# Optimization experiments

Hardware: AMD Instinct MI355X
Metric: run time of the kernel (lower is better)

Reference implementation:

```python
import jax, jax.numpy as jnp
import numpy as np

EPS = 1e-12  # matches torch.nn.functional.normalize default eps


def setup_inputs() -> dict:
    key = jax.random.key(0)
    k_x, k_org = jax.random.split(key)
    batch, times, d = 32, 256, 2048
    x = jax.random.normal(k_x, (batch, d, d), dtype=jnp.float32)
    # org.data.normal_(mean=0, std=0.1)
    org = 0.1 * jax.random.normal(k_org, (times, d), dtype=jnp.float32)
    return {"x": x, "org": org}


def reference(x, org):
    # F.normalize(org, dim=-1): divide each row by max(||row||_2, eps)
    norm = jnp.linalg.norm(org, axis=-1, keepdims=True)
    o = org / jnp.maximum(norm, EPS)  # (times, d)
    # Original: m = o_a (x) o_a  (rank-1 projectors, (times,d,d));
    #           y = einsum('abc,dce->dabe', m, x); trace = einsum('abcc->ab', y)
    # Algebraically: trace[batch, time] = sum_{b,c} o[a,b] * o[a,c] * x[d,c,b]
    # i.e. the quadratic form o^T x^T o per (batch, time) pair -- same math,
    # without materializing the (batch, times, d, d) intermediate.
    trace = jnp.einsum('ab,ac,dcb->da', o, o, x)  # (batch, times)
    return trace
```

## Files before the change

### kernel.cpp

```cpp
#include <hip/hip_runtime.h>
#include <hip/hip_bf16.h>

#define DDIM 2048
#define TTIMES 256
#define NT 64
#define THREADS 512

typedef __attribute__((ext_vector_type(8))) short short8;
typedef __attribute__((ext_vector_type(4))) float f32x4;

using gvoid = const __attribute__((address_space(1))) void;
using svoid = __attribute__((address_space(3))) void;

__device__ __forceinline__ void gld16(const void* g, void* l) {
    __builtin_amdgcn_global_load_lds((gvoid*)g, (svoid*)l, 16, 0, 0);
}

__device__ __forceinline__ ushort f2bf(float f) {
    union { float f; unsigned int u; } v; v.f = f;
    unsigned int u = v.u;
    unsigned int r = (u + 0x7FFFu + ((u >> 16) & 1u)) >> 16;
    return (ushort)r;
}
__device__ __forceinline__ float bf2f(ushort u) {
    union { unsigned int u; float f; } v; v.u = ((unsigned int)u) << 16;
    return v.f;
}
__device__ __forceinline__ short cvt1(float f) {
    union { __hip_bfloat16 h; ushort u; } cv;
    cv.h = __float2bfloat16(f);
    return (short)cv.u;
}

__global__ void norm_rows(const float* __restrict__ org, ushort* __restrict__ obf) {
    const int a   = blockIdx.x;
    const int tid = threadIdx.x;
    const float* row = org + (size_t)a * DDIM;
    float4 v0 = ((const float4*)row)[tid * 2];
    float4 v1 = ((const float4*)row)[tid * 2 + 1];
    float s = v0.x*v0.x + v0.y*v0.y + v0.z*v0.z + v0.w*v0.w
            + v1.x*v1.x + v1.y*v1.y + v1.z*v1.z + v1.w*v1.w;
    #pragma unroll
    for (int off = 1; off < 64; off <<= 1) s += __shfl_xor(s, off);
    __shared__ float wsum[4];
    const int lane = tid & 63, w = tid >> 6;
    if (lane == 0) wsum[w] = s;
    __syncthreads();
    const float tot = wsum[0] + wsum[1] + wsum[2] + wsum[3];
    const float scale = 1.0f / fmaxf(sqrtf(tot), 1e-12f);
    union { ushort u[8]; uint4 v; } pk;
    pk.u[0] = f2bf(v0.x * scale); pk.u[1] = f2bf(v0.y * scale);
    pk.u[2] = f2bf(v0.z * scale); pk.u[3] = f2bf(v0.w * scale);
    pk.u[4] = f2bf(v1.x * scale); pk.u[5] = f2bf(v1.y * scale);
    pk.u[6] = f2bf(v1.z * scale); pk.u[7] = f2bf(v1.w * scale);
    ((uint4*)(obf + (size_t)a * DDIM))[tid] = pk.v;
}

__global__ __launch_bounds__(THREADS, 4) void gemm_trace(
    const float* __restrict__ x, const ushort* __restrict__ obf,
    float* __restrict__ part)
{
    __shared__ __align__(16) char Ab[3][16384];
    __shared__ __align__(16) char Bb[2][16384];

    const int tid  = threadIdx.x;
    const int lane = tid & 63;
    const int wid  = tid >> 6;
    const int wm   = wid >> 2;
    const int wn   = wid & 3;
    const int rb   = blockIdx.x;
    const int d    = blockIdx.y;
    const int t0   = (d * 16 + rb) & (NT - 1);
#define W(n) ((t0 + (n)) & (NT - 1))

    const char* ab = (const char*)(x + (size_t)d * DDIM * DDIM + (size_t)rb * 128 * DDIM);
    const char* bb = (const char*)obf;

    const int ar0 = tid >> 3,         aq0 = ((tid & 7) ^ (ar0 & 7)) * 16;
    const int ar1 = (tid + 512) >> 3, aq1 = (((tid + 512) & 7) ^ (ar1 & 7)) * 16;
    const int br0 = tid >> 2,         bq0 = ((tid & 3) ^ (br0 & 3)) * 16;
    const int br1 = (tid + 512) >> 2, bq1 = (((tid + 512) & 3) ^ (br1 & 3)) * 16;

    const char* as0 = ab + (size_t)ar0 * (DDIM * 4) + aq0;
    const char* as1 = ab + (size_t)ar1 * (DDIM * 4) + aq1;
    const char* bs0 = bb + (size_t)br0 * (DDIM * 2) + bq0;
    const char* bs1 = bb + (size_t)br1 * (DDIM * 2) + bq1;

#define STAGE_A(t, buf) do {                                  \
    gld16(as0 + (t) * 128, &Ab[buf][tid * 16]);               \
    gld16(as1 + (t) * 128, &Ab[buf][(tid + 512) * 16]);       \
} while (0)
#define STAGE_B(t, buf) do {                                  \
    gld16(bs0 + (t) * 64,  &Bb[buf][tid * 16]);               \
    gld16(bs1 + (t) * 64,  &Bb[buf][(tid + 512) * 16]);       \
} while (0)

    const int lr = lane & 15;
    const int lq = lane >> 4;

    int aoff0[4], aoff1[4], boff[4];
    #pragma unroll
    for (int mi = 0; mi < 4; ++mi) {
        const int r = wm * 64 + mi * 16 + lr;
        aoff0[mi] = r * 128 + ((2 * lq)     ^ (r & 7)) * 16;
        aoff1[mi] = r * 128 + ((2 * lq + 1) ^ (r & 7)) * 16;
    }
    #pragma unroll
    for (int ni = 0; ni < 4; ++ni) {
        const int rt = wn * 64 + ni * 16 + lr;
        boff[ni] = rt * 64 + (lq ^ (rt & 3)) * 16;
    }

    f32x4 acc[4][4];
    #pragma unroll
    for (int mi = 0; mi < 4; ++mi)
        #pragma unroll
        for (int ni = 0; ni < 4; ++ni)
            acc[mi][ni] = (f32x4){0.f, 0.f, 0.f, 0.f};

#define COMPUTE(abuf, bbuf) do {                                            \
    short8 af[4], bfr[4];                                                   \
    _Pragma("unroll")                                                       \
    for (int mi = 0; mi < 4; ++mi) {                                        \
        const float4 lo = *(const float4*)&Ab[abuf][aoff0[mi]];             \
        const float4 hi = *(const float4*)&Ab[abuf][aoff1[mi]];             \
        short8 a8;                                                          \
        a8[0] = cvt1(lo.x); a8[1] = cvt1(lo.y);                             \
        a8[2] = cvt1(lo.z); a8[3] = cvt1(lo.w);                             \
        a8[4] = cvt1(hi.x); a8[5] = cvt1(hi.y);                             \
        a8[6] = cvt1(hi.z); a8[7] = cvt1(hi.w);                             \
        af[mi] = a8;                                                        \
    }                                                                       \
    _Pragma("unroll")                                                       \
    for (int ni = 0; ni < 4; ++ni)                                          \
        bfr[ni] = *(const short8*)&Bb[bbuf][boff[ni]];                      \
    _Pragma("unroll")                                                       \
    for (int mi = 0; mi < 4; ++mi)                                          \
        _Pragma("unroll")                                                   \
        for (int ni = 0; ni < 4; ++ni)                                      \
            acc[mi][ni] = __builtin_amdgcn_mfma_f32_16x16x32_bf16(          \
                af[mi], bfr[ni], acc[mi][ni], 0, 0, 0);                     \
} while (0)

#define VMW(n) do {                                                         \
    asm volatile("s_waitcnt vmcnt(" #n ")" ::: "memory");                   \
    __builtin_amdgcn_sched_barrier(0); } while (0)
#define SBAR do {                                                           \
    __builtin_amdgcn_sched_barrier(0);                                      \
    asm volatile("s_waitcnt lgkmcnt(0)" ::: "memory");                      \
    __builtin_amdgcn_s_barrier();                                           \
    __builtin_amdgcn_sched_barrier(0); } while (0)

    STAGE_A(W(0), 0);
    STAGE_B(W(0), 0);
    STAGE_A(W(1), 1);

    int abf = 0;
    #pragma unroll 1
    for (int t = 0; t < NT - 1; ++t) {
        VMW(2);
        SBAR;
        STAGE_B(W(t + 1), (t + 1) & 1);
        if (t + 2 < NT) {
            int ab2 = abf + 2; if (ab2 >= 3) ab2 -= 3;
            STAGE_A(W(t + 2), ab2);
        }
        COMPUTE(abf, t & 1);
        ++abf; if (abf == 3) abf = 0;
    }
    VMW(0);
    SBAR;
    COMPUTE(abf, (NT - 1) & 1);
    __syncthreads();

#undef W
#undef STAGE_A
#undef STAGE_B
#undef COMPUTE
#undef VMW
#undef SBAR

    float* plds = (float*)&Ab[0][0];

    #pragma unroll
    for (int ni = 0; ni < 4; ++ni) {
        const int a_idx = wn * 64 + ni * 16 + lr;
        float ps = 0.f;
        #pragma unroll
        for (int mi = 0; mi < 4; ++mi) {
            const int bg = rb * 128 + wm * 64 + mi * 16 + lq * 4;
            const ushort4 w = *(const ushort4*)(obf + (size_t)a_idx * DDIM + bg);
            ps += bf2f(w.x) * acc[mi][ni][0];
            ps += bf2f(w.y) * acc[mi][ni][1];
            ps += bf2f(w.z) * acc[mi][ni][2];
            ps += bf2f(w.w) * acc[mi][ni][3];
        }
        ps += __shfl_xor(ps, 16);
        ps += __shfl_xor(ps, 32);
        if (lane < 16) plds[wm * 256 + a_idx] = ps;
    }
    __syncthreads();
    if (tid < 256)
        part[((size_t)d * 16 + rb) * TTIMES + tid] = plds[tid] + plds[256 + tid];
}

__global__ void reduce_part(const float* __restrict__ part, float* __restrict__ out) {
    const int d = blockIdx.x;
    const int a = threadIdx.x;
    float s = 0.f;
    #pragma unroll
    for (int rb = 0; rb < 16; ++rb)
        s += part[((size_t)d * 16 + rb) * TTIMES + a];
    out[(size_t)d * TTIMES + a] = s;
}

extern "C" void kernel_launch(void* const* d_in, const int* in_sizes, int n_in,
                              void* d_out, int out_size, void* d_ws, size_t ws_size,
                              hipStream_t stream) {
    const float* x   = (const float*)d_in[0];
    const float* org = (const float*)d_in[1];
    float* out = (float*)d_out;

    ushort* obf = (ushort*)d_ws;
    float*  prt = (float*)((char*)d_ws + (1 << 20));

    norm_rows<<<dim3(TTIMES), dim3(256), 0, stream>>>(org, obf);
    gemm_trace<<<dim3(16, 32), dim3(THREADS), 0, stream>>>(x, obf, prt);
    reduce_part<<<dim3(32), dim3(256), 0, stream>>>(prt, out);
}
```

Before: 129.9 us.

## Double block size to 1024 threads with 64-wide K tiles for x

Moves the GEMM kernel to 1024 threads (16 waves, 4x4 wave grid, 32 rows per wave) and stages x in 64-column K tiles (32KB per buffer), so each A tile is split into two 32-wide K sub-steps that share one B stage per sub-step. This halves the number of A pipeline iterations and barrier waits per A load, and changes the B swizzle. The intent is to use more waves per CU and fewer sync points for the fp32 x stream. The cost is more LDS per block (about 128KB), which may limit residency, plus an extra barrier per sub-step. The launch bounds min-block hint and host launch configuration are not visible.

```diff
diff --git a/kernel.cpp b/kernel.cpp
--- a/kernel.cpp
+++ b/kernel.cpp
@@ -3,8 +3,8 @@
 
 #define DDIM 2048
 #define TTIMES 256
-#define NT 64
-#define THREADS 512
+#define NTA 32
+#define THREADS 1024
 
 typedef __attribute__((ext_vector_type(8))) short short8;
 typedef __attribute__((ext_vector_type(4))) float f32x4;
@@ -60,7 +60,7 @@
     const float* __restrict__ x, const ushort* __restrict__ obf,
     float* __restrict__ part)
 {
-    __shared__ __align__(16) char Ab[3][16384];
+    __shared__ __align__(16) char Ab[3][32768];
     __shared__ __align__(16) char Bb[2][16384];
 
     const int tid  = threadIdx.x;
@@ -70,60 +70,62 @@
     const int wn   = wid & 3;
     const int rb   = blockIdx.x;
     const int d    = blockIdx.y;
-    const int t0   = (d * 16 + rb) & (NT - 1);
-#define W(n) ((t0 + (n)) & (NT - 1))
+    const int T0   = (d * 16 + rb) & (NTA - 1);
+#define WT(n) ((T0 + (n)) & (NTA - 1))
 
     const char* ab = (const char*)(x + (size_t)d * DDIM * DDIM + (size_t)rb * 128 * DDIM);
     const char* bb = (const char*)obf;
 
-    const int ar0 = tid >> 3,         aq0 = ((tid & 7) ^ (ar0 & 7)) * 16;
-    const int ar1 = (tid + 512) >> 3, aq1 = (((tid + 512) & 7) ^ (ar1 & 7)) * 16;
-    const int br0 = tid >> 2,         bq0 = ((tid & 3) ^ (br0 & 3)) * 16;
-    const int br1 = (tid + 512) >> 2, bq1 = (((tid + 512) & 3) ^ (br1 & 3)) * 16;
-
+    const int ac0 = tid,        ar0 = ac0 >> 4, aq0 = ((ac0 & 15) ^ (ar0 & 7)) * 16;
+    const int ac1 = tid + 1024, ar1 = ac1 >> 4, aq1 = ((ac1 & 15) ^ (ar1 & 7)) * 16;
     const char* as0 = ab + (size_t)ar0 * (DDIM * 4) + aq0;
     const char* as1 = ab + (size_t)ar1 * (DDIM * 4) + aq1;
-    const char* bs0 = bb + (size_t)br0 * (DDIM * 2) + bq0;
-    const char* bs1 = bb + (size_t)br1 * (DDIM * 2) + bq1;
-
-#define STAGE_A(t, buf) do {                                  \
-    gld16(as0 + (t) * 128, &Ab[buf][tid * 16]);               \
-    gld16(as1 + (t) * 128, &Ab[buf][(tid + 512) * 16]);       \
+
+    const int brw = tid >> 2;
+    const char* bsr = bb + (size_t)brw * (DDIM * 2)
+                    + (((tid & 3) ^ ((brw >> 1) & 3)) * 16);
+
+#define STAGE_A(T, buf) do {                                  \
+    gld16(as0 + (size_t)(T) * 256, &Ab[buf][ac0 * 16]);       \
+    gld16(as1 + (size_t)(T) * 256, &Ab[buf][ac1 * 16]);       \
 } while (0)
-#define STAGE_B(t, buf) do {                                  \
-    gld16(bs0 + (t) * 64,  &Bb[buf][tid * 16]);               \
-    gld16(bs1 + (t) * 64,  &Bb[buf][(tid + 512) * 16]);       \
+#define STAGE_B(g, buf) do {                                  \
+    gld16(bsr + (size_t)(g) * 64, &Bb[buf][tid * 16]);        \
 } while (0)
 
     const int lr = lane & 15;
     const int lq = lane >> 4;
 
-    int aoff0[4], aoff1[4], boff[4];
-    #pragma unroll
-    for (int mi = 0; mi < 4; ++mi) {
-        const int r = wm * 64 + mi * 16 + lr;
-        aoff0[mi] = r * 128 + ((2 * lq)     ^ (r & 7)) * 16;
-        aoff1[mi] = r * 128 + ((2 * lq + 1) ^ (r & 7)) * 16;
-    }
+    int arow[2], arx[2];
+    #pragma unroll
+    for (int mi = 0; mi < 2; ++mi) {
+        const int ra = wm * 32 + mi * 16 + lr;
+        arow[mi] = ra * 256;
+        arx[mi]  = ra & 7;
+    }
+    int boff[4];
     #pragma unroll
     for (int ni = 0; ni < 4; ++ni) {
         const int rt = wn * 64 + ni * 16 + lr;
-        boff[ni] = rt * 64 + (lq ^ (rt & 3)) * 16;
-    }
-
-    f32x4 acc[4][4];
-    #pragma unroll
-    for (int mi = 0; mi < 4; ++mi)
+        boff[ni] = rt * 64 + ((lq ^ ((rt >> 1) & 3)) * 16);
+    }
+
+    f32x4 acc[2][4];
+    #pragma unroll
+    for (int mi = 0; mi < 2; ++mi)
         #pragma unroll
         for (int ni = 0; ni < 4; ++ni)
             acc[mi][ni] = (f32x4){0.f, 0.f, 0.f, 0.f};
 
-#define COMPUTE(abuf, bbuf) do {                                            \
-    short8 af[4], bfr[4];                                                   \
+#define COMPUTE(abuf, ksub, bbuf) do {                                      \
+    short8 af[2], bfr[4];                                                   \
     _Pragma("unroll")                                                       \
-    for (int mi = 0; mi < 4; ++mi) {                                        \
-        const float4 lo = *(const float4*)&Ab[abuf][aoff0[mi]];             \
-        const float4 hi = *(const float4*)&Ab[abuf][aoff1[mi]];             \
+    for (int mi = 0; mi < 2; ++mi) {                                        \
+        const int q0_ = (ksub) * 8 + lq * 2;                                \
+        const float4 lo = *(const float4*)                                  \
+            &Ab[abuf][arow[mi] + ((q0_)     ^ arx[mi]) * 16];               \
+        const float4 hi = *(const float4*)                                  \
+            &Ab[abuf][arow[mi] + ((q0_ + 1) ^ arx[mi]) * 16];               \
         short8 a8;                                                          \
         a8[0] = cvt1(lo.x); a8[1] = cvt1(lo.y);                             \
         a8[2] = cvt1(lo.z); a8[3] = cvt1(lo.w);                             \
@@ -135,7 +137,7 @@
     for (int ni = 0; ni < 4; ++ni)                                          \
         bfr[ni] = *(const short8*)&Bb[bbuf][boff[ni]];                      \
     _Pragma("unroll")                                                       \
-    for (int mi = 0; mi < 4; ++mi)                                          \
+    for (int mi = 0; mi < 2; ++mi)                                          \
         _Pragma("unroll")                                                   \
         for (int ni = 0; ni < 4; ++ni)                                      \
             acc[mi][ni] = __builtin_amdgcn_mfma_f32_16x16x32_bf16(          \
@@ -151,29 +153,38 @@
     __builtin_amdgcn_s_barrier();                                           \
     __builtin_amdgcn_sched_barrier(0); } while (0)
 
-    STAGE_A(W(0), 0);
-    STAGE_B(W(0), 0);
-    STAGE_A(W(1), 1);
+    STAGE_A(WT(0), 0);
+    STAGE_B(WT(0) * 2 + 0, 0);
+    STAGE_A(WT(1), 1);
 
     int abf = 0;
     #pragma unroll 1
-    for (int t = 0; t < NT - 1; ++t) {
-        VMW(2);
+    for (int T = 0; T < NTA - 1; ++T) {
+        VMW(0);
         SBAR;
-        STAGE_B(W(t + 1), (t + 1) & 1);
-        if (t + 2 < NT) {
+        STAGE_B(WT(T) * 2 + 1, 1);
+        if (T + 2 < NTA) {
             int ab2 = abf + 2; if (ab2 >= 3) ab2 -= 3;
-            STAGE_A(W(t + 2), ab2);
+            STAGE_A(WT(T + 2), ab2);
         }
-        COMPUTE(abf, t & 1);
+        COMPUTE(abf, 0, 0);
+        if (T + 2 < NTA) { VMW(2); }
+        else             { VMW(0); }
+        SBAR;
+        STAGE_B(WT(T + 1) * 2 + 0, 0);
+        COMPUTE(abf, 1, 1);
         ++abf; if (abf == 3) abf = 0;
     }
     VMW(0);
     SBAR;
-    COMPUTE(abf, (NT - 1) & 1);
+    STAGE_B(WT(NTA - 1) * 2 + 1, 1);
+    COMPUTE(abf, 0, 0);
+    VMW(0);
+    SBAR;
+    COMPUTE(abf, 1, 1);
     __syncthreads();
 
-#undef W
+#undef WT
 #undef STAGE_A
 #undef STAGE_B
 #undef COMPUTE
@@ -187,8 +198,8 @@
         const int a_idx = wn * 64 + ni * 16 + lr;
         float ps = 0.f;
         #pragma unroll
-        for (int mi = 0; mi < 4; ++mi) {
-            const int bg = rb * 128 + wm * 64 + mi * 16 + lq * 4;
+        for (int mi = 0; mi < 2; ++mi) {
+            const int bg = rb * 128 + wm * 32 + mi * 16 + lq * 4;
             const ushort4 w = *(const ushort4*)(obf + (size_t)a_idx * DDIM + bg);
             ps += bf2f(w.x) * acc[mi][ni][0];
             ps += bf2f(w.y) * acc[mi][ni][1];
@@ -201,7 +212,8 @@
     }
     __syncthreads();
     if (tid < 256)
-        part[((size_t)d * 16 + rb) * TTIMES + tid] = plds[tid] + plds[256 + tid];
+        part[((size_t)d * 16 + rb) * TTIMES + tid] =
+            plds[tid] + plds[256 + tid] + plds[512 + tid] + plds[768 + tid];
 }
 
 __global__ void reduce_part(const float* __restrict__ part, float* __restrict__ out) {
```

New measurement: 167.6 us. +29.0%, slower.

## Double the per-block row tile to 256 rows and halve the grid

Applied to the files above, without the earlier changes.

Each block now covers 256 rows of x instead of 128. The warp grid changes to 4x2, and each warp computes 64x128 with 32 accumulator tiles. This halves how many times each block reloads the shared bf16 o matrix and halves the partial sums written and reduced. The cost is twice the shared memory for the A buffers, more registers, launch bounds lowered to 2 blocks per SM, and only 256 blocks in the grid, which can lower occupancy and latency hiding. The kernel is mainly bound by streaming x, so the saving on B traffic may be small.

```diff
diff --git a/kernel.cpp b/kernel.cpp
--- a/kernel.cpp
+++ b/kernel.cpp
@@ -56,49 +56,55 @@
     ((uint4*)(obf + (size_t)a * DDIM))[tid] = pk.v;
 }
 
-__global__ __launch_bounds__(THREADS, 4) void gemm_trace(
+__global__ __launch_bounds__(THREADS, 2) void gemm_trace(
     const float* __restrict__ x, const ushort* __restrict__ obf,
     float* __restrict__ part)
 {
-    __shared__ __align__(16) char Ab[3][16384];
+    __shared__ __align__(16) char Ab[3][32768];
     __shared__ __align__(16) char Bb[2][16384];
 
     const int tid  = threadIdx.x;
     const int lane = tid & 63;
     const int wid  = tid >> 6;
-    const int wm   = wid >> 2;
-    const int wn   = wid & 3;
+    const int wm   = wid >> 1;
+    const int wn   = wid & 1;
     const int rb   = blockIdx.x;
     const int d    = blockIdx.y;
-    const int t0   = (d * 16 + rb) & (NT - 1);
+    const int t0   = (d * 8 + rb) & (NT - 1);
 #define W(n) ((t0 + (n)) & (NT - 1))
 
-    const char* ab = (const char*)(x + (size_t)d * DDIM * DDIM + (size_t)rb * 128 * DDIM);
+    const char* ab = (const char*)(x + (size_t)d * DDIM * DDIM + (size_t)rb * 256 * DDIM);
     const char* bb = (const char*)obf;
 
-    const int ar0 = tid >> 3,         aq0 = ((tid & 7) ^ (ar0 & 7)) * 16;
-    const int ar1 = (tid + 512) >> 3, aq1 = (((tid + 512) & 7) ^ (ar1 & 7)) * 16;
-    const int br0 = tid >> 2,         bq0 = ((tid & 3) ^ (br0 & 3)) * 16;
-    const int br1 = (tid + 512) >> 2, bq1 = (((tid + 512) & 3) ^ (br1 & 3)) * 16;
-
-    const char* as0 = ab + (size_t)ar0 * (DDIM * 4) + aq0;
-    const char* as1 = ab + (size_t)ar1 * (DDIM * 4) + aq1;
-    const char* bs0 = bb + (size_t)br0 * (DDIM * 2) + bq0;
-    const char* bs1 = bb + (size_t)br1 * (DDIM * 2) + bq1;
+    const int ac0 = tid,        ar0_ = ac0 >> 3, aq0 = ((ac0 & 7) ^ (ar0_ & 7)) * 16;
+    const int ac1 = tid + 512,  ar1_ = ac1 >> 3, aq1 = ((ac1 & 7) ^ (ar1_ & 7)) * 16;
+    const int ac2 = tid + 1024, ar2_ = ac2 >> 3, aq2 = ((ac2 & 7) ^ (ar2_ & 7)) * 16;
+    const int ac3 = tid + 1536, ar3_ = ac3 >> 3, aq3 = ((ac3 & 7) ^ (ar3_ & 7)) * 16;
+    const char* as0 = ab + (size_t)ar0_ * (DDIM * 4) + aq0;
+    const char* as1 = ab + (size_t)ar1_ * (DDIM * 4) + aq1;
+    const char* as2 = ab + (size_t)ar2_ * (DDIM * 4) + aq2;
+    const char* as3 = ab + (size_t)ar3_ * (DDIM * 4) + aq3;
+
+    const int bc0 = tid,       br0_ = bc0 >> 2, bq0 = ((bc0 & 3) ^ (br0_ & 3)) * 16;
+    const int bc1 = tid + 512, br1_ = bc1 >> 2, bq1 = ((bc1 & 3) ^ (br1_ & 3)) * 16;
+    const char* bs0 = bb + (size_t)br0_ * (DDIM * 2) + bq0;
+    const char* bs1 = bb + (size_t)br1_ * (DDIM * 2) + bq1;
 
 #define STAGE_A(t, buf) do {                                  \
-    gld16(as0 + (t) * 128, &Ab[buf][tid * 16]);               \
-    gld16(as1 + (t) * 128, &Ab[buf][(tid + 512) * 16]);       \
+    gld16(as0 + (t) * 128, &Ab[buf][ac0 * 16]);               \
+    gld16(as1 + (t) * 128, &Ab[buf][ac1 * 16]);               \
+    gld16(as2 + (t) * 128, &Ab[buf][ac2 * 16]);               \
+    gld16(as3 + (t) * 128, &Ab[buf][ac3 * 16]);               \
 } while (0)
 #define STAGE_B(t, buf) do {                                  \
-    gld16(bs0 + (t) * 64,  &Bb[buf][tid * 16]);               \
-    gld16(bs1 + (t) * 64,  &Bb[buf][(tid + 512) * 16]);       \
+    gld16(bs0 + (t) * 64,  &Bb[buf][bc0 * 16]);               \
+    gld16(bs1 + (t) * 64,  &Bb[buf][bc1 * 16]);               \
 } while (0)
 
     const int lr = lane & 15;
     const int lq = lane >> 4;
 
-    int aoff0[4], aoff1[4], boff[4];
+    int aoff0[4], aoff1[4], boff[8];
     #pragma unroll
     for (int mi = 0; mi < 4; ++mi) {
         const int r = wm * 64 + mi * 16 + lr;
@@ -106,20 +112,20 @@
         aoff1[mi] = r * 128 + ((2 * lq + 1) ^ (r & 7)) * 16;
     }
     #pragma unroll
-    for (int ni = 0; ni < 4; ++ni) {
-        const int rt = wn * 64 + ni * 16 + lr;
+    for (int ni = 0; ni < 8; ++ni) {
+        const int rt = wn * 128 + ni * 16 + lr;
         boff[ni] = rt * 64 + (lq ^ (rt & 3)) * 16;
     }
 
-    f32x4 acc[4][4];
+    f32x4 acc[4][8];
     #pragma unroll
     for (int mi = 0; mi < 4; ++mi)
         #pragma unroll
-        for (int ni = 0; ni < 4; ++ni)
+        for (int ni = 0; ni < 8; ++ni)
             acc[mi][ni] = (f32x4){0.f, 0.f, 0.f, 0.f};
 
 #define COMPUTE(abuf, bbuf) do {                                            \
-    short8 af[4], bfr[4];                                                   \
+    short8 af[4], bfr[8];                                                   \
     _Pragma("unroll")                                                       \
     for (int mi = 0; mi < 4; ++mi) {                                        \
         const float4 lo = *(const float4*)&Ab[abuf][aoff0[mi]];             \
@@ -132,12 +138,12 @@
         af[mi] = a8;                                                        \
     }                                                                       \
     _Pragma("unroll")                                                       \
-    for (int ni = 0; ni < 4; ++ni)                                          \
+    for (int ni = 0; ni < 8; ++ni)                                          \
         bfr[ni] = *(const short8*)&Bb[bbuf][boff[ni]];                      \
     _Pragma("unroll")                                                       \
     for (int mi = 0; mi < 4; ++mi)                                          \
         _Pragma("unroll")                                                   \
-        for (int ni = 0; ni < 4; ++ni)                                      \
+        for (int ni = 0; ni < 8; ++ni)                                      \
             acc[mi][ni] = __builtin_amdgcn_mfma_f32_16x16x32_bf16(          \
                 af[mi], bfr[ni], acc[mi][ni], 0, 0, 0);                     \
 } while (0)
@@ -158,7 +164,7 @@
     int abf = 0;
     #pragma unroll 1
     for (int t = 0; t < NT - 1; ++t) {
-        VMW(2);
+        VMW(4);
         SBAR;
         STAGE_B(W(t + 1), (t + 1) & 1);
         if (t + 2 < NT) {
@@ -183,12 +189,12 @@
     float* plds = (float*)&Ab[0][0];
 
     #pragma unroll
-    for (int ni = 0; ni < 4; ++ni) {
-        const int a_idx = wn * 64 + ni * 16 + lr;
+    for (int ni = 0; ni < 8; ++ni) {
+        const int a_idx = wn * 128 + ni * 16 + lr;
         float ps = 0.f;
         #pragma unroll
         for (int mi = 0; mi < 4; ++mi) {
-            const int bg = rb * 128 + wm * 64 + mi * 16 + lq * 4;
+            const int bg = rb * 256 + wm * 64 + mi * 16 + lq * 4;
             const ushort4 w = *(const ushort4*)(obf + (size_t)a_idx * DDIM + bg);
             ps += bf2f(w.x) * acc[mi][ni][0];
             ps += bf2f(w.y) * acc[mi][ni][1];
@@ -201,7 +207,8 @@
     }
     __syncthreads();
     if (tid < 256)
-        part[((size_t)d * 16 + rb) * TTIMES + tid] = plds[tid] + plds[256 + tid];
+        part[((size_t)d * 8 + rb) * TTIMES + tid] =
+            plds[tid] + plds[256 + tid] + plds[512 + tid] + plds[768 + tid];
 }
 
 __global__ void reduce_part(const float* __restrict__ part, float* __restrict__ out) {
@@ -209,8 +216,8 @@
     const int a = threadIdx.x;
     float s = 0.f;
     #pragma unroll
-    for (int rb = 0; rb < 16; ++rb)
-        s += part[((size_t)d * 16 + rb) * TTIMES + a];
+    for (int rb = 0; rb < 8; ++rb)
+        s += part[((size_t)d * 8 + rb) * TTIMES + a];
     out[(size_t)d * TTIMES + a] = s;
 }
 
@@ -225,6 +232,6 @@
     float*  prt = (float*)((char*)d_ws + (1 << 20));
 
     norm_rows<<<dim3(TTIMES), dim3(256), 0, stream>>>(org, obf);
-    gemm_trace<<<dim3(16, 32), dim3(THREADS), 0, stream>>>(x, obf, prt);
+    gemm_trace<<<dim3(8, 32), dim3(THREADS), 0, stream>>>(x, obf, prt);
     reduce_part<<<dim3(32), dim3(256), 0, stream>>>(prt, out);
 }
```

Result: slower. 139.5 us (+7.3%).

## Convert A tile to bf16 once in registers before LDS, double-buffer K=64 steps

Applied to the files above, without the earlier changes.

Instead of async-copying fp32 x tiles into LDS and having each wave convert them to bf16 on every fragment read, threads now load fp32 x into registers, convert once, and write bf16 into a half-size LDS buffer. The K loop now steps 64 per iteration, with two B sub-stages per A stage. This removes redundant per-wave conversions and halves A LDS footprint and read traffic. In exchange A loads become synchronous register loads with extra barriers per iteration, which may expose global latency.

```diff
diff --git a/kernel.cpp b/kernel.cpp
--- a/kernel.cpp
+++ b/kernel.cpp
@@ -3,7 +3,7 @@
 
 #define DDIM 2048
 #define TTIMES 256
-#define NT 64
+#define NTA 32
 #define THREADS 512
 
 typedef __attribute__((ext_vector_type(8))) short short8;
@@ -26,10 +26,10 @@
     union { unsigned int u; float f; } v; v.u = ((unsigned int)u) << 16;
     return v.f;
 }
-__device__ __forceinline__ short cvt1(float f) {
+__device__ __forceinline__ ushort cvt1(float f) {
     union { __hip_bfloat16 h; ushort u; } cv;
     cv.h = __float2bfloat16(f);
-    return (short)cv.u;
+    return cv.u;
 }
 
 __global__ void norm_rows(const float* __restrict__ org, ushort* __restrict__ obf) {
@@ -60,8 +60,8 @@
     const float* __restrict__ x, const ushort* __restrict__ obf,
     float* __restrict__ part)
 {
-    __shared__ __align__(16) char Ab[3][16384];
-    __shared__ __align__(16) char Bb[2][16384];
+    __shared__ __align__(16) ushort Ab[2][8192];
+    __shared__ __align__(16) char   Bb[2][16384];
 
     const int tid  = threadIdx.x;
     const int lane = tid & 63;
@@ -70,40 +70,26 @@
     const int wn   = wid & 3;
     const int rb   = blockIdx.x;
     const int d    = blockIdx.y;
-    const int t0   = (d * 16 + rb) & (NT - 1);
-#define W(n) ((t0 + (n)) & (NT - 1))
-
-    const char* ab = (const char*)(x + (size_t)d * DDIM * DDIM + (size_t)rb * 128 * DDIM);
-    const char* bb = (const char*)obf;
-
-    const int ar0 = tid >> 3,         aq0 = ((tid & 7) ^ (ar0 & 7)) * 16;
-    const int ar1 = (tid + 512) >> 3, aq1 = (((tid + 512) & 7) ^ (ar1 & 7)) * 16;
-    const int br0 = tid >> 2,         bq0 = ((tid & 3) ^ (br0 & 3)) * 16;
-    const int br1 = (tid + 512) >> 2, bq1 = (((tid + 512) & 3) ^ (br1 & 3)) * 16;
-
-    const char* as0 = ab + (size_t)ar0 * (DDIM * 4) + aq0;
-    const char* as1 = ab + (size_t)ar1 * (DDIM * 4) + aq1;
-    const char* bs0 = bb + (size_t)br0 * (DDIM * 2) + bq0;
-    const char* bs1 = bb + (size_t)br1 * (DDIM * 2) + bq1;
-
-#define STAGE_A(t, buf) do {                                  \
-    gld16(as0 + (t) * 128, &Ab[buf][tid * 16]);               \
-    gld16(as1 + (t) * 128, &Ab[buf][(tid + 512) * 16]);       \
-} while (0)
-#define STAGE_B(t, buf) do {                                  \
-    gld16(bs0 + (t) * 64,  &Bb[buf][tid * 16]);               \
-    gld16(bs1 + (t) * 64,  &Bb[buf][(tid + 512) * 16]);       \
-} while (0)
-
-    const int lr = lane & 15;
-    const int lq = lane >> 4;
-
-    int aoff0[4], aoff1[4], boff[4];
+    const int T0   = (d * 16 + rb) & (NTA - 1);
+#define W(n) ((T0 + (n)) & (NTA - 1))
+
+    const int arow = tid >> 2, ac = tid & 3;
+    const float* asrc = x + (size_t)d * DDIM * DDIM
+                          + (size_t)(rb * 128 + arow) * DDIM + ac * 16;
+    const int awoff0 = arow * 64 + (((ac * 2)     ^ (arow & 7)) * 8);
+    const int awoff1 = arow * 64 + (((ac * 2 + 1) ^ (arow & 7)) * 8);
+
+    const char* bs0 = (const char*)obf + (size_t)(tid >> 2) * (DDIM * 2)
+                    + ((tid & 3) ^ ((tid >> 2) & 3)) * 16;
+    const char* bs1 = bs0 + (size_t)128 * (DDIM * 2);
+
+    const int lr = lane & 15, lq = lane >> 4;
+    int abase[4], arx[4], boff[4];
     #pragma unroll
     for (int mi = 0; mi < 4; ++mi) {
         const int r = wm * 64 + mi * 16 + lr;
-        aoff0[mi] = r * 128 + ((2 * lq)     ^ (r & 7)) * 16;
-        aoff1[mi] = r * 128 + ((2 * lq + 1) ^ (r & 7)) * 16;
+        abase[mi] = r * 64;
+        arx[mi]   = r & 7;
     }
     #pragma unroll
     for (int ni = 0; ni < 4; ++ni) {
@@ -118,19 +104,40 @@
         for (int ni = 0; ni < 4; ++ni)
             acc[mi][ni] = (f32x4){0.f, 0.f, 0.f, 0.f};
 
-#define COMPUTE(abuf, bbuf) do {                                            \
+    float4 a0, a1, a2, a3;
+
+#define ALOAD(T) do {                                                       \
+    const float* p_ = asrc + (size_t)(W(T)) * 64;                           \
+    a0 = *(const float4*)p_;       a1 = *(const float4*)(p_ + 4);           \
+    a2 = *(const float4*)(p_ + 8); a3 = *(const float4*)(p_ + 12);          \
+} while (0)
+
+#define WRITE_A(buf) do {                                                   \
+    union { ushort u[8]; uint4 v; } pk_;                                    \
+    pk_.u[0] = cvt1(a0.x); pk_.u[1] = cvt1(a0.y);                           \
+    pk_.u[2] = cvt1(a0.z); pk_.u[3] = cvt1(a0.w);                           \
+    pk_.u[4] = cvt1(a1.x); pk_.u[5] = cvt1(a1.y);                           \
+    pk_.u[6] = cvt1(a1.z); pk_.u[7] = cvt1(a1.w);                           \
+    *(uint4*)&Ab[buf][awoff0] = pk_.v;                                      \
+    pk_.u[0] = cvt1(a2.x); pk_.u[1] = cvt1(a2.y);                           \
+    pk_.u[2] = cvt1(a2.z); pk_.u[3] = cvt1(a2.w);                           \
+    pk_.u[4] = cvt1(a3.x); pk_.u[5] = cvt1(a3.y);                           \
+    pk_.u[6] = cvt1(a3.z); pk_.u[7] = cvt1(a3.w);                           \
+    *(uint4*)&Ab[buf][awoff1] = pk_.v;                                      \
+} while (0)
+
+#define STAGE_B(T, ksub, buf) do {                                          \
+    const size_t off_ = (size_t)(W(T)) * 128 + (ksub) * 64;                 \
+    gld16(bs0 + off_, &Bb[buf][tid * 16]);                                  \
+    gld16(bs1 + off_, &Bb[buf][8192 + tid * 16]);                           \
+} while (0)
+
+#define COMPUTE(abuf, ksub, bbuf) do {                                      \
     short8 af[4], bfr[4];                                                   \
     _Pragma("unroll")                                                       \
-    for (int mi = 0; mi < 4; ++mi) {                                        \
-        const float4 lo = *(const float4*)&Ab[abuf][aoff0[mi]];             \
-        const float4 hi = *(const float4*)&Ab[abuf][aoff1[mi]];             \
-        short8 a8;                                                          \
-        a8[0] = cvt1(lo.x); a8[1] = cvt1(lo.y);                             \
-        a8[2] = cvt1(lo.z); a8[3] = cvt1(lo.w);                             \
-        a8[4] = cvt1(hi.x); a8[5] = cvt1(hi.y);                             \
-        a8[6] = cvt1(hi.z); a8[7] = cvt1(hi.w);                             \
-        af[mi] = a8;                                                        \
-    }                                                                       \
+    for (int mi = 0; mi < 4; ++mi)                                          \
+        af[mi] = *(const short8*)                                           \
+            &Ab[abuf][abase[mi] + ((((ksub) * 4 + lq) ^ arx[mi]) * 8)];     \
     _Pragma("unroll")                                                       \
     for (int ni = 0; ni < 4; ++ni)                                          \
         bfr[ni] = *(const short8*)&Bb[bbuf][boff[ni]];                      \
@@ -151,30 +158,37 @@
     __builtin_amdgcn_s_barrier();                                           \
     __builtin_amdgcn_sched_barrier(0); } while (0)
 
-    STAGE_A(W(0), 0);
-    STAGE_B(W(0), 0);
-    STAGE_A(W(1), 1);
-
-    int abf = 0;
+    ALOAD(0);
+    WRITE_A(0);
+    STAGE_B(0, 0, 0);
+    ALOAD(1);
+
     #pragma unroll 1
-    for (int t = 0; t < NT - 1; ++t) {
-        VMW(2);
+    for (int T = 0; T < NTA - 1; ++T) {
+        const int ab_ = T & 1;
+        VMW(4);
         SBAR;
-        STAGE_B(W(t + 1), (t + 1) & 1);
-        if (t + 2 < NT) {
-            int ab2 = abf + 2; if (ab2 >= 3) ab2 -= 3;
-            STAGE_A(W(t + 2), ab2);
-        }
-        COMPUTE(abf, t & 1);
-        ++abf; if (abf == 3) abf = 0;
+        STAGE_B(T, 1, 1);
+        COMPUTE(ab_, 0, 0);
+        VMW(0);
+        SBAR;
+        STAGE_B(T + 1, 0, 0);
+        WRITE_A(ab_ ^ 1);
+        if (T + 2 < NTA) ALOAD(T + 2);
+        COMPUTE(ab_, 1, 1);
     }
     VMW(0);
     SBAR;
-    COMPUTE(abf, (NT - 1) & 1);
+    STAGE_B(NTA - 1, 1, 1);
+    COMPUTE(1, 0, 0);
+    VMW(0);
+    SBAR;
+    COMPUTE(1, 1, 1);
     __syncthreads();
 
 #undef W
-#undef STAGE_A
+#undef ALOAD
+#undef WRITE_A
 #undef STAGE_B
 #undef COMPUTE
 #undef VMW
```

Result: slower. 138.6 us (+6.6%).
